# Performance work log

Hardware: AMD Instinct MI355X
Metric: run time of the kernel (lower is better)

The kernel has to match this reference:

```python
import math
import jax, jax.numpy as jnp
import numpy as np

B, T, D, N = 4, 4096, 2048, 32
_EPS_NORM = 1e-12  # F.normalize eps
_C = math.sqrt(2.0 / math.pi)


def setup_inputs() -> dict:
    key = jax.random.key(0)
    k1, k2 = jax.random.split(key)
    x = jax.random.normal(k1, (B, T, D), dtype=jnp.float32)
    buf = jax.random.normal(k2, (N, D), dtype=jnp.float32)
    mask = jnp.ones((N,), dtype=bool)  # fully-filled ring buffer (steady state)
    log_alpha = jnp.asarray(math.log(math.exp(0.5) - 1.0), dtype=jnp.float32)
    log_tau = jnp.asarray(math.log(2.0), dtype=jnp.float32)
    return {"x": x, "buf": buf, "mask": mask, "log_alpha": log_alpha, "log_tau": log_tau}


def _gelu_tanh(x):
    return 0.5 * x * (1.0 + jnp.tanh(_C * (x + 0.044715 * x * x * x)))


def reference(x, buf, mask, log_alpha, log_tau):
    # x: [B,T,D], buf: [N,D] (non-differentiable ring-buffer state), mask: [N] bool
    alpha = jax.nn.softplus(log_alpha)
    tau = jnp.exp(log_tau)
    y = _gelu_tanh(x)                                   # [B,T,D]

    # current episode mean (detached in torch)
    m_curr = jax.lax.stop_gradient(y.reshape(-1, y.shape[-1]).mean(0))  # [D]

    # cosine similarity of buffer rows vs current mean (F.normalize semantics)
    m_norm = m_curr / jnp.maximum(jnp.linalg.norm(m_curr), _EPS_NORM)   # [D]
    b_norm = buf / jnp.maximum(
        jnp.linalg.norm(buf, axis=-1, keepdims=True), _EPS_NORM)        # [N,D]
    sims = jnp.where(mask, b_norm @ m_norm, -1.0)                       # [N]
    nearest_ep = jax.lax.stop_gradient(buf[jnp.argmax(sims)])           # [D]

    # unbiased std over filled buffer rows (mask-weighted, matches torch .std(0))
    w = mask.astype(buf.dtype)[:, None]                                  # [N,1]
    n = w.sum()
    mu = (buf * w).sum(0) / n                                            # [D]
    var = (w * (buf - mu) ** 2).sum(0) / (n - 1.0)
    buf_std = jnp.clip(jnp.sqrt(var), 0.0001, None)                      # [D]

    dev = (y - nearest_ep) / (buf_std + 1e-05)
    fam = jnp.exp(-tau * dev * dev)
    gate = jnp.clip(1.0 - alpha * fam, 0.05, 1.05)
    return y * gate
```

## Files before the change

kernel.cpp:

```cpp
#include <hip/hip_runtime.h>
#include <math.h>

#define DIM  2048
#define ROWS 16384
#define NBUF 32
#define NREP 64

#define WS_REP   0
#define WS_INV   (NREP * DIM)
#define WS_NE    (WS_INV + DIM)
#define WS_ALPHA (WS_NE + DIM)
#define WS_TAU   (WS_ALPHA + 1)

__device__ __forceinline__ float fast_tanh(float z) {
    float az = fabsf(z);
    float e  = __expf(2.0f * az);
    float t  = 1.0f - 2.0f / (e + 1.0f);
    return copysignf(t, z);
}

__device__ __forceinline__ float gelu_tanh(float x) {
    float x3 = x * x * x;
    float z  = 0.7978845608028654f * (x + 0.044715f * x3);
    return 0.5f * x * (1.0f + fast_tanh(z));
}

__global__ __launch_bounds__(256) void zero_kernel(float* __restrict__ ws) {
    const int i = blockIdx.x * 256 + threadIdx.x;
    float4 z = {0.f, 0.f, 0.f, 0.f};
    ((float4*)(ws + WS_REP))[i] = z;
}

__global__ __launch_bounds__(256) void colsum_kernel(const float* __restrict__ x,
                                                     float* __restrict__ ws) {
    const int t  = threadIdx.x;
    const int rg = blockIdx.x >> 1;
    const int h  = blockIdx.x & 1;
    const float4* base = (const float4*)x + (size_t)rg * 16 * 512 + h * 256 + t;

    float4 v[16];
    #pragma unroll
    for (int r = 0; r < 16; ++r) v[r] = base[(size_t)r * 512];

    __builtin_amdgcn_sched_barrier(0);

    float4 a = {0.f, 0.f, 0.f, 0.f};
    #pragma unroll
    for (int r = 0; r < 16; ++r) {
        a.x += gelu_tanh(v[r].x);
        a.y += gelu_tanh(v[r].y);
        a.z += gelu_tanh(v[r].z);
        a.w += gelu_tanh(v[r].w);
    }
    float* rep = ws + WS_REP + (size_t)(rg & (NREP - 1)) * DIM + h * 1024;
    const int c0 = t * 4;
    atomicAdd(&rep[c0 + 0], a.x);
    atomicAdd(&rep[c0 + 1], a.y);
    atomicAdd(&rep[c0 + 2], a.z);
    atomicAdd(&rep[c0 + 3], a.w);
}

__global__ __launch_bounds__(1024) void mid_kernel(const float* __restrict__ buf,
                                                   const float* __restrict__ log_alpha,
                                                   const float* __restrict__ log_tau,
                                                   float* __restrict__ ws) {
    __shared__ float mean_lds[DIM];
    __shared__ float red[1024];
    __shared__ float dots[NBUF];
    __shared__ float bsqs[NBUF];
    __shared__ int ksh;
    const int t = threadIdx.x;

    float msq_local = 0.f;
    for (int c = t; c < DIM; c += 1024) {
        float s = 0.f;
        #pragma unroll 8
        for (int r = 0; r < NREP; ++r) s += ws[WS_REP + (size_t)r * DIM + c];
        float mean = s * (1.0f / (float)ROWS);
        mean_lds[c] = mean;
        msq_local += mean * mean;

        float bs = 0.f, bss = 0.f;
        #pragma unroll 8
        for (int n = 0; n < NBUF; ++n) {
            float v = buf[(size_t)n * DIM + c];
            bs += v; bss += v * v;
        }
        float mu  = bs * (1.0f / (float)NBUF);
        float var = (bss - (float)NBUF * mu * mu) * (1.0f / (float)(NBUF - 1));
        var = fmaxf(var, 0.f);
        float sd = fmaxf(sqrtf(var), 1e-4f);
        ws[WS_INV + c] = 1.0f / (sd + 1e-5f);
    }
    red[t] = msq_local; __syncthreads();
    for (int s = 512; s > 0; s >>= 1) { if (t < s) red[t] += red[t + s]; __syncthreads(); }
    const float msq = red[0];

    const int w = t >> 6, lane = t & 63;
    for (int n = w; n < NBUF; n += 16) {
        float d = 0.f, q = 0.f;
        for (int c = lane; c < DIM; c += 64) {
            float bv = buf[(size_t)n * DIM + c];
            d += bv * mean_lds[c];
            q += bv * bv;
        }
        for (int off = 32; off > 0; off >>= 1) {
            d += __shfl_down(d, off);
            q += __shfl_down(q, off);
        }
        if (lane == 0) { dots[n] = d; bsqs[n] = q; }
    }
    __syncthreads();

    if (t == 0) {
        float mnorm = fmaxf(sqrtf(msq), 1e-12f);
        float best = -1e30f; int bi = 0;
        for (int n = 0; n < NBUF; ++n) {
            float bn  = fmaxf(sqrtf(bsqs[n]), 1e-12f);
            float sim = dots[n] / (bn * mnorm);
            if (sim > best) { best = sim; bi = n; }
        }
        ksh = bi;
        float la = log_alpha[0];
        ws[WS_ALPHA] = (la > 20.0f) ? la : log1pf(expf(la));
        ws[WS_TAU]   = expf(log_tau[0]);
    }
    __syncthreads();

    const int k = ksh;
    for (int c = t; c < DIM; c += 1024) ws[WS_NE + c] = buf[(size_t)k * DIM + c];
}

__global__ __launch_bounds__(256) void gate_kernel(const float* __restrict__ x,
                                                   const float* __restrict__ ws,
                                                   float* __restrict__ out) {
    const float alpha = ws[WS_ALPHA];
    const float tau   = ws[WS_TAU];
    const size_t gtid   = (size_t)blockIdx.x * 256 + threadIdx.x;
    const size_t stride = (size_t)gridDim.x * 256;
    const size_t nvec   = (size_t)ROWS * DIM / 4;

    const int colv = (int)(gtid & 511);
    const float4 nv = ((const float4*)(ws + WS_NE))[colv];
    const float4 iv = ((const float4*)(ws + WS_INV))[colv];
    const float4* xv4 = (const float4*)x;
    float4* ov4       = (float4*)out;

    for (size_t i = gtid; i < nvec; i += 2 * stride) {
        float4 xa = xv4[i];
        float4 xb = xv4[i + stride];
        float4 oa, ob;
        {
            float y = gelu_tanh(xa.x); float dv = (y - nv.x) * iv.x;
            float g = fminf(fmaxf(1.0f - alpha * __expf(-tau * dv * dv), 0.05f), 1.05f);
            oa.x = y * g;
        }
        {
            float y = gelu_tanh(xa.y); float dv = (y - nv.y) * iv.y;
            float g = fminf(fmaxf(1.0f - alpha * __expf(-tau * dv * dv), 0.05f), 1.05f);
            oa.y = y * g;
        }
        {
            float y = gelu_tanh(xa.z); float dv = (y - nv.z) * iv.z;
            float g = fminf(fmaxf(1.0f - alpha * __expf(-tau * dv * dv), 0.05f), 1.05f);
            oa.z = y * g;
        }
        {
            float y = gelu_tanh(xa.w); float dv = (y - nv.w) * iv.w;
            float g = fminf(fmaxf(1.0f - alpha * __expf(-tau * dv * dv), 0.05f), 1.05f);
            oa.w = y * g;
        }
        {
            float y = gelu_tanh(xb.x); float dv = (y - nv.x) * iv.x;
            float g = fminf(fmaxf(1.0f - alpha * __expf(-tau * dv * dv), 0.05f), 1.05f);
            ob.x = y * g;
        }
        {
            float y = gelu_tanh(xb.y); float dv = (y - nv.y) * iv.y;
            float g = fminf(fmaxf(1.0f - alpha * __expf(-tau * dv * dv), 0.05f), 1.05f);
            ob.y = y * g;
        }
        {
            float y = gelu_tanh(xb.z); float dv = (y - nv.z) * iv.z;
            float g = fminf(fmaxf(1.0f - alpha * __expf(-tau * dv * dv), 0.05f), 1.05f);
            ob.z = y * g;
        }
        {
            float y = gelu_tanh(xb.w); float dv = (y - nv.w) * iv.w;
            float g = fminf(fmaxf(1.0f - alpha * __expf(-tau * dv * dv), 0.05f), 1.05f);
            ob.w = y * g;
        }
        ov4[i] = oa;
        ov4[i + stride] = ob;
    }
}

extern "C" void kernel_launch(void* const* d_in, const int* in_sizes, int n_in,
                              void* d_out, int out_size, void* d_ws, size_t ws_size,
                              hipStream_t stream) {
    const float* x   = (const float*)d_in[0];
    const float* buf = (const float*)d_in[1];
    const float* la  = (const float*)d_in[3];
    const float* lt  = (const float*)d_in[4];
    float* out = (float*)d_out;
    float* ws  = (float*)d_ws;

    hipLaunchKernelGGL(zero_kernel,   dim3(128),  dim3(256),  0, stream, ws);
    hipLaunchKernelGGL(colsum_kernel, dim3(2048), dim3(256),  0, stream, x, ws);
    hipLaunchKernelGGL(mid_kernel,    dim3(1),    dim3(1024), 0, stream, buf, la, lt, ws);
    hipLaunchKernelGGL(gate_kernel,   dim3(4096), dim3(256),  0, stream, x, ws, out);
}
```

Baseline: 124.3 us.

## Restructure colsum, mid and gate kernels with paired float4 access and rcp tanh

Replaces the divide in the tanh approximation with a hardware reciprocal. The column-sum and gate kernels now give each thread two adjacent float4 columns over a fixed row block, which halves the grid and drops the grid-stride loop. The single-block mid kernel is vectorised with float4 loads and splits threads between the mean reduction and the buffer statistics. Each thread now moves 32 contiguous bytes, which changes the coalescing pattern and lowers occupancy per launch. The colsum kernel also loses its explicit load-all-then-compute scheduling barrier.

```diff
diff --git a/kernel.cpp b/kernel.cpp
--- a/kernel.cpp
+++ b/kernel.cpp
@@ -15,7 +15,8 @@
 __device__ __forceinline__ float fast_tanh(float z) {
     float az = fabsf(z);
     float e  = __expf(2.0f * az);
-    float t  = 1.0f - 2.0f / (e + 1.0f);
+    float r  = __builtin_amdgcn_rcpf(e + 1.0f);
+    float t  = 1.0f - 2.0f * r;
     return copysignf(t, z);
 }
 
@@ -33,76 +34,94 @@
 
 __global__ __launch_bounds__(256) void colsum_kernel(const float* __restrict__ x,
                                                      float* __restrict__ ws) {
-    const int t  = threadIdx.x;
-    const int rg = blockIdx.x >> 1;
-    const int h  = blockIdx.x & 1;
-    const float4* base = (const float4*)x + (size_t)rg * 16 * 512 + h * 256 + t;
-
-    float4 v[16];
-    #pragma unroll
-    for (int r = 0; r < 16; ++r) v[r] = base[(size_t)r * 512];
-
-    __builtin_amdgcn_sched_barrier(0);
-
-    float4 a = {0.f, 0.f, 0.f, 0.f};
+    const int t = threadIdx.x;
+    const int b = blockIdx.x;
+    const float4* base = (const float4*)x + (size_t)b * 16 * 512 + 2 * t;
+    float4 a0 = {0.f, 0.f, 0.f, 0.f};
+    float4 a1 = {0.f, 0.f, 0.f, 0.f};
     #pragma unroll
     for (int r = 0; r < 16; ++r) {
-        a.x += gelu_tanh(v[r].x);
-        a.y += gelu_tanh(v[r].y);
-        a.z += gelu_tanh(v[r].z);
-        a.w += gelu_tanh(v[r].w);
-    }
-    float* rep = ws + WS_REP + (size_t)(rg & (NREP - 1)) * DIM + h * 1024;
-    const int c0 = t * 4;
-    atomicAdd(&rep[c0 + 0], a.x);
-    atomicAdd(&rep[c0 + 1], a.y);
-    atomicAdd(&rep[c0 + 2], a.z);
-    atomicAdd(&rep[c0 + 3], a.w);
+        float4 v0 = base[r * 512];
+        float4 v1 = base[r * 512 + 1];
+        a0.x += gelu_tanh(v0.x); a0.y += gelu_tanh(v0.y);
+        a0.z += gelu_tanh(v0.z); a0.w += gelu_tanh(v0.w);
+        a1.x += gelu_tanh(v1.x); a1.y += gelu_tanh(v1.y);
+        a1.z += gelu_tanh(v1.z); a1.w += gelu_tanh(v1.w);
+    }
+    float* rep = ws + WS_REP + (size_t)(b & (NREP - 1)) * DIM;
+    const int c0 = t * 8;
+    atomicAdd(&rep[c0 + 0], a0.x);
+    atomicAdd(&rep[c0 + 1], a0.y);
+    atomicAdd(&rep[c0 + 2], a0.z);
+    atomicAdd(&rep[c0 + 3], a0.w);
+    atomicAdd(&rep[c0 + 4], a1.x);
+    atomicAdd(&rep[c0 + 5], a1.y);
+    atomicAdd(&rep[c0 + 6], a1.z);
+    atomicAdd(&rep[c0 + 7], a1.w);
 }
 
 __global__ __launch_bounds__(1024) void mid_kernel(const float* __restrict__ buf,
                                                    const float* __restrict__ log_alpha,
                                                    const float* __restrict__ log_tau,
                                                    float* __restrict__ ws) {
-    __shared__ float mean_lds[DIM];
+    __shared__ float4 mean4[512];
     __shared__ float red[1024];
     __shared__ float dots[NBUF];
     __shared__ float bsqs[NBUF];
-    __shared__ int ksh;
+    __shared__ int   ksh;
     const int t = threadIdx.x;
-
-    float msq_local = 0.f;
-    for (int c = t; c < DIM; c += 1024) {
-        float s = 0.f;
-        #pragma unroll 8
-        for (int r = 0; r < NREP; ++r) s += ws[WS_REP + (size_t)r * DIM + c];
-        float mean = s * (1.0f / (float)ROWS);
-        mean_lds[c] = mean;
-        msq_local += mean * mean;
-
-        float bs = 0.f, bss = 0.f;
-        #pragma unroll 8
+    const float4* rep4 = (const float4*)(ws + WS_REP);
+    const float4* buf4 = (const float4*)buf;
+
+    float msq_part = 0.f;
+    if (t < 512) {
+        float4 acc = {0.f, 0.f, 0.f, 0.f};
+        for (int r = 0; r < NREP; ++r) {
+            float4 v = rep4[(size_t)r * 512 + t];
+            acc.x += v.x; acc.y += v.y; acc.z += v.z; acc.w += v.w;
+        }
+        const float inv_rows = 1.0f / (float)ROWS;
+        float4 m = { acc.x * inv_rows, acc.y * inv_rows,
+                     acc.z * inv_rows, acc.w * inv_rows };
+        mean4[t] = m;
+        msq_part = m.x * m.x + m.y * m.y + m.z * m.z + m.w * m.w;
+    } else {
+        const int j = t - 512;
+        float4 bs  = {0.f, 0.f, 0.f, 0.f};
+        float4 bss = {0.f, 0.f, 0.f, 0.f};
         for (int n = 0; n < NBUF; ++n) {
-            float v = buf[(size_t)n * DIM + c];
-            bs += v; bss += v * v;
-        }
-        float mu  = bs * (1.0f / (float)NBUF);
-        float var = (bss - (float)NBUF * mu * mu) * (1.0f / (float)(NBUF - 1));
-        var = fmaxf(var, 0.f);
-        float sd = fmaxf(sqrtf(var), 1e-4f);
-        ws[WS_INV + c] = 1.0f / (sd + 1e-5f);
-    }
-    red[t] = msq_local; __syncthreads();
+            float4 v = buf4[(size_t)n * 512 + j];
+            bs.x += v.x;       bs.y += v.y;       bs.z += v.z;       bs.w += v.w;
+            bss.x += v.x*v.x;  bss.y += v.y*v.y;  bss.z += v.z*v.z;  bss.w += v.w*v.w;
+        }
+        const float invn = 1.0f / (float)NBUF, invn1 = 1.0f / (float)(NBUF - 1);
+        float4 iv;
+        {
+            float mu = bs.x*invn, va = fmaxf((bss.x - NBUF*mu*mu)*invn1, 0.f);
+            iv.x = 1.0f / (fmaxf(sqrtf(va), 1e-4f) + 1e-5f);
+            mu = bs.y*invn; va = fmaxf((bss.y - NBUF*mu*mu)*invn1, 0.f);
+            iv.y = 1.0f / (fmaxf(sqrtf(va), 1e-4f) + 1e-5f);
+            mu = bs.z*invn; va = fmaxf((bss.z - NBUF*mu*mu)*invn1, 0.f);
+            iv.z = 1.0f / (fmaxf(sqrtf(va), 1e-4f) + 1e-5f);
+            mu = bs.w*invn; va = fmaxf((bss.w - NBUF*mu*mu)*invn1, 0.f);
+            iv.w = 1.0f / (fmaxf(sqrtf(va), 1e-4f) + 1e-5f);
+        }
+        ((float4*)(ws + WS_INV))[j] = iv;
+    }
+    red[t] = msq_part; __syncthreads();
     for (int s = 512; s > 0; s >>= 1) { if (t < s) red[t] += red[t + s]; __syncthreads(); }
     const float msq = red[0];
 
     const int w = t >> 6, lane = t & 63;
     for (int n = w; n < NBUF; n += 16) {
         float d = 0.f, q = 0.f;
-        for (int c = lane; c < DIM; c += 64) {
-            float bv = buf[(size_t)n * DIM + c];
-            d += bv * mean_lds[c];
-            q += bv * bv;
+        #pragma unroll
+        for (int k = 0; k < 8; ++k) {
+            int j = k * 64 + lane;
+            float4 v = buf4[(size_t)n * 512 + j];
+            float4 m = mean4[j];
+            d += v.x*m.x + v.y*m.y + v.z*m.z + v.w*m.w;
+            q += v.x*v.x + v.y*v.y + v.z*v.z + v.w*v.w;
         }
         for (int off = 32; off > 0; off >>= 1) {
             d += __shfl_down(d, off);
@@ -127,71 +146,51 @@
     }
     __syncthreads();
 
-    const int k = ksh;
-    for (int c = t; c < DIM; c += 1024) ws[WS_NE + c] = buf[(size_t)k * DIM + c];
+    if (t < 512) ((float4*)(ws + WS_NE))[t] = buf4[(size_t)ksh * 512 + t];
 }
 
 __global__ __launch_bounds__(256) void gate_kernel(const float* __restrict__ x,
                                                    const float* __restrict__ ws,
                                                    float* __restrict__ out) {
+    const int t = threadIdx.x;
+    const int b = blockIdx.x;
     const float alpha = ws[WS_ALPHA];
     const float tau   = ws[WS_TAU];
-    const size_t gtid   = (size_t)blockIdx.x * 256 + threadIdx.x;
-    const size_t stride = (size_t)gridDim.x * 256;
-    const size_t nvec   = (size_t)ROWS * DIM / 4;
-
-    const int colv = (int)(gtid & 511);
-    const float4 nv = ((const float4*)(ws + WS_NE))[colv];
-    const float4 iv = ((const float4*)(ws + WS_INV))[colv];
-    const float4* xv4 = (const float4*)x;
-    float4* ov4       = (float4*)out;
-
-    for (size_t i = gtid; i < nvec; i += 2 * stride) {
-        float4 xa = xv4[i];
-        float4 xb = xv4[i + stride];
+    const float4 nv0 = ((const float4*)(ws + WS_NE))[2 * t];
+    const float4 nv1 = ((const float4*)(ws + WS_NE))[2 * t + 1];
+    const float4 iv0 = ((const float4*)(ws + WS_INV))[2 * t];
+    const float4 iv1 = ((const float4*)(ws + WS_INV))[2 * t + 1];
+
+    const float4* base = (const float4*)x + (size_t)b * 8 * 512 + 2 * t;
+    float4* ov         = (float4*)out     + (size_t)b * 8 * 512 + 2 * t;
+
+    #pragma unroll
+    for (int r = 0; r < 8; ++r) {
+        float4 xa = base[r * 512];
+        float4 xb = base[r * 512 + 1];
         float4 oa, ob;
         {
-            float y = gelu_tanh(xa.x); float dv = (y - nv.x) * iv.x;
-            float g = fminf(fmaxf(1.0f - alpha * __expf(-tau * dv * dv), 0.05f), 1.05f);
-            oa.x = y * g;
+            float y = gelu_tanh(xa.x); float dv = (y - nv0.x) * iv0.x;
+            oa.x = y * fminf(fmaxf(1.0f - alpha * __expf(-tau * dv * dv), 0.05f), 1.05f);
+            y = gelu_tanh(xa.y); dv = (y - nv0.y) * iv0.y;
+            oa.y = y * fminf(fmaxf(1.0f - alpha * __expf(-tau * dv * dv), 0.05f), 1.05f);
+            y = gelu_tanh(xa.z); dv = (y - nv0.z) * iv0.z;
+            oa.z = y * fminf(fmaxf(1.0f - alpha * __expf(-tau * dv * dv), 0.05f), 1.05f);
+            y = gelu_tanh(xa.w); dv = (y - nv0.w) * iv0.w;
+            oa.w = y * fminf(fmaxf(1.0f - alpha * __expf(-tau * dv * dv), 0.05f), 1.05f);
         }
         {
-            float y = gelu_tanh(xa.y); float dv = (y - nv.y) * iv.y;
-            float g = fminf(fmaxf(1.0f - alpha * __expf(-tau * dv * dv), 0.05f), 1.05f);
-            oa.y = y * g;
-        }
-        {
-            float y = gelu_tanh(xa.z); float dv = (y - nv.z) * iv.z;
-            float g = fminf(fmaxf(1.0f - alpha * __expf(-tau * dv * dv), 0.05f), 1.05f);
-            oa.z = y * g;
-        }
-        {
-            float y = gelu_tanh(xa.w); float dv = (y - nv.w) * iv.w;
-            float g = fminf(fmaxf(1.0f - alpha * __expf(-tau * dv * dv), 0.05f), 1.05f);
-            oa.w = y * g;
-        }
-        {
-            float y = gelu_tanh(xb.x); float dv = (y - nv.x) * iv.x;
-            float g = fminf(fmaxf(1.0f - alpha * __expf(-tau * dv * dv), 0.05f), 1.05f);
-            ob.x = y * g;
-        }
-        {
-            float y = gelu_tanh(xb.y); float dv = (y - nv.y) * iv.y;
-            float g = fminf(fmaxf(1.0f - alpha * __expf(-tau * dv * dv), 0.05f), 1.05f);
-            ob.y = y * g;
-        }
-        {
-            float y = gelu_tanh(xb.z); float dv = (y - nv.z) * iv.z;
-            float g = fminf(fmaxf(1.0f - alpha * __expf(-tau * dv * dv), 0.05f), 1.05f);
-            ob.z = y * g;
-        }
-        {
-            float y = gelu_tanh(xb.w); float dv = (y - nv.w) * iv.w;
-            float g = fminf(fmaxf(1.0f - alpha * __expf(-tau * dv * dv), 0.05f), 1.05f);
-            ob.w = y * g;
-        }
-        ov4[i] = oa;
-        ov4[i + stride] = ob;
+            float y = gelu_tanh(xb.x); float dv = (y - nv1.x) * iv1.x;
+            ob.x = y * fminf(fmaxf(1.0f - alpha * __expf(-tau * dv * dv), 0.05f), 1.05f);
+            y = gelu_tanh(xb.y); dv = (y - nv1.y) * iv1.y;
+            ob.y = y * fminf(fmaxf(1.0f - alpha * __expf(-tau * dv * dv), 0.05f), 1.05f);
+            y = gelu_tanh(xb.z); dv = (y - nv1.z) * iv1.z;
+            ob.z = y * fminf(fmaxf(1.0f - alpha * __expf(-tau * dv * dv), 0.05f), 1.05f);
+            y = gelu_tanh(xb.w); dv = (y - nv1.w) * iv1.w;
+            ob.w = y * fminf(fmaxf(1.0f - alpha * __expf(-tau * dv * dv), 0.05f), 1.05f);
+        }
+        ov[r * 512]     = oa;
+        ov[r * 512 + 1] = ob;
     }
 }
 
@@ -206,7 +205,7 @@
     float* ws  = (float*)d_ws;
 
     hipLaunchKernelGGL(zero_kernel,   dim3(128),  dim3(256),  0, stream, ws);
-    hipLaunchKernelGGL(colsum_kernel, dim3(2048), dim3(256),  0, stream, x, ws);
+    hipLaunchKernelGGL(colsum_kernel, dim3(1024), dim3(256),  0, stream, x, ws);
     hipLaunchKernelGGL(mid_kernel,    dim3(1),    dim3(1024), 0, stream, buf, la, lt, ws);
-    hipLaunchKernelGGL(gate_kernel,   dim3(4096), dim3(256),  0, stream, x, ws, out);
-}
+    hipLaunchKernelGGL(gate_kernel,   dim3(2048), dim3(256),  0, stream, x, ws, out);
+}
```

Result: slower. 147.6 us (+18.7%).
